# Optimization experiments

Measured on AMD Instinct MI355X. Metric: run time of the kernel, lower is better.

The kernel has to match this reference:

```python
import jax, jax.numpy as jnp
import numpy as np

B, T, V, D, H = 64, 256, 32000, 512, 1024  # batch, seq_len, vocab, word_dim, hidden/embed_dim


def setup_inputs() -> dict:
    key = jax.random.key(0)
    ks = jax.random.split(key, 7)
    tokens = jax.random.randint(ks[0], (B, T), 0, V, dtype=jnp.int64)
    lengths = jnp.maximum(1, jax.random.randint(ks[1], (B,), 0, T + 1, dtype=jnp.int64))
    embedding = jax.random.normal(ks[2], (V, D), dtype=jnp.float32) * 0.05
    W_ih = jax.random.normal(ks[3], (4 * H, D), dtype=jnp.float32) * 0.05
    W_hh = jax.random.normal(ks[4], (4 * H, H), dtype=jnp.float32) * 0.05
    b_ih = jax.random.normal(ks[5], (4 * H,), dtype=jnp.float32) * 0.05
    b_hh = jax.random.normal(ks[6], (4 * H,), dtype=jnp.float32) * 0.05
    return {"tokens": tokens, "lengths": lengths, "embedding": embedding,
            "W_ih": W_ih, "W_hh": W_hh, "b_ih": b_ih, "b_hh": b_hh}


def _lstm_encode(tokens, lengths, embedding, W_ih, W_hh, b_ih, b_hh):
    b, t = tokens.shape
    x = embedding[tokens]                       # [B, T, D] token embedding lookup
    xs = jnp.swapaxes(x, 0, 1)                  # [T, B, D] time-major for scan
    mask = jnp.arange(t)[:, None] < lengths[None, :]  # [T, B] valid-step mask

    h0 = jnp.zeros((b, W_hh.shape[1]), dtype=x.dtype)
    c0 = jnp.zeros_like(h0)

    def step(carry, inp):
        h, c = carry
        xt, mt = inp
        # torch LSTMCell: gates = x W_ih^T + b_ih + h W_hh^T + b_hh, chunk order i, f, g, o
        gates = xt @ W_ih.T + b_ih + h @ W_hh.T + b_hh
        i, f, g, o = jnp.split(gates, 4, axis=-1)
        i = jax.nn.sigmoid(i)
        f = jax.nn.sigmoid(f)
        g = jnp.tanh(g)
        o = jax.nn.sigmoid(o)
        c_new = f * c + i * g
        h_new = o * jnp.tanh(c_new)
        m = mt[:, None]
        # freeze state past each sequence's length -> final h is h at t = length
        h = jnp.where(m, h_new, h)
        c = jnp.where(m, c_new, c)
        return (h, c), None

    (h, c), _ = jax.lax.scan(step, (h0, c0), (xs, mask))
    return h  # [B, H] final hidden state


def reference(tokens, lengths, embedding, W_ih, W_hh, b_ih, b_hh):
    return _lstm_encode(tokens, lengths, embedding, W_ih, W_hh, b_ih, b_hh)
```

## Files before the change

kernel.cpp:

```cpp
#include <hip/hip_runtime.h>


typedef __attribute__((ext_vector_type(8))) short    sh8;
typedef __attribute__((ext_vector_type(4))) float    fx4;
typedef __attribute__((ext_vector_type(4))) unsigned ux4;

__device__ __forceinline__ unsigned short f2bf(float x) {
  unsigned u = __builtin_bit_cast(unsigned, x);
  return (unsigned short)((u + 0x7FFFu + ((u >> 16) & 1u)) >> 16);
}
__device__ __forceinline__ float bf2f(unsigned short s) {
  return __builtin_bit_cast(float, (unsigned)s << 16);
}
__device__ __forceinline__ float sigm(float x) { return 1.0f / (1.0f + __expf(-x)); }
__device__ __forceinline__ float tanh_(float x) { return 2.0f / (1.0f + __expf(-2.0f * x)) - 1.0f; }

__device__ __forceinline__ void ld_sc(sh8& v, const void* p) {
  asm volatile("global_load_dwordx4 %0, %1, off sc0 sc1" : "=v"(v) : "v"(p) : "memory");
}
__device__ __forceinline__ void ld_sc4u(ux4& v, const void* p) {
  asm volatile("global_load_dwordx4 %0, %1, off sc0 sc1" : "=v"(v) : "v"(p) : "memory");
}
__device__ __forceinline__ void st_sc2(void* p, unsigned v) {
  asm volatile("global_store_short %0, %1, off sc0 sc1" :: "v"(p), "v"(v) : "memory");
}
__device__ __forceinline__ void st_sc4(void* p, unsigned v) {
  asm volatile("global_store_dword %0, %1, off sc0 sc1" :: "v"(p), "v"(v) : "memory");
}


__global__ void k_convert(const float* __restrict__ src, ushort* __restrict__ dst, int n4) {
  int i = blockIdx.x * blockDim.x + threadIdx.x;
  int stride = gridDim.x * blockDim.x;
  for (; i < n4; i += stride) {
    float4 v = ((const float4*)src)[i];
    ((ushort4*)dst)[i] = make_ushort4(f2bf(v.x), f2bf(v.y), f2bf(v.z), f2bf(v.w));
  }
}

__global__ void k_bias(const float* __restrict__ bi, const float* __restrict__ bh,
                       float* __restrict__ bias) {
  int i = blockIdx.x * 256 + threadIdx.x;
  if (i < 4096) bias[i] = bi[i] + bh[i];
}

__global__ void k_gather(const int* __restrict__ tokens, const float* __restrict__ emb,
                         ushort* __restrict__ X) {
  int m = blockIdx.x * 4 + (threadIdx.x >> 6);
  int lane = threadIdx.x & 63;
  int b = m & 63, tt = m >> 6;
  int tok = tokens[b * 256 + tt];
  const float4* src = (const float4*)(emb + (size_t)tok * 512);
  ushort4* dst = (ushort4*)(X + (size_t)m * 512);
#pragma unroll
  for (int i = 0; i < 2; ++i) {
    float4 v = src[lane + i * 64];
    dst[lane + i * 64] = make_ushort4(f2bf(v.x), f2bf(v.y), f2bf(v.z), f2bf(v.w));
  }
}


__global__ __launch_bounds__(256) void k1_gemm(const ushort* __restrict__ X,
                                               const ushort* __restrict__ W,
                                               const float* __restrict__ bias,
                                               ushort* __restrict__ Xg) {
  __shared__ __align__(16) char As[128 * 128];
  __shared__ __align__(16) char Bs[128 * 128];
  const int tid = threadIdx.x, lane = tid & 63, wid = tid >> 6;
  const int wm = wid & 1, wn = wid >> 1;
  const int m0 = blockIdx.y * 128, n0 = blockIdx.x * 128;

  fx4 acc[4][4] = {};

  for (int kt = 0; kt < 8; ++kt) {
    if (kt) __syncthreads();
#pragma unroll
    for (int i = 0; i < 4; ++i) {
      int a = tid * 16 + i * 4096;
      int row = a >> 7, inrow = a & 127;
      int dsa = (row << 7) + (inrow ^ ((row & 7) << 4));
      sh8 va = *(const sh8*)((const char*)X + (size_t)(m0 + row) * 1024 + kt * 128 + inrow);
      *(sh8*)(As + dsa) = va;
      sh8 vb = *(const sh8*)((const char*)W + (size_t)(n0 + row) * 1024 + kt * 128 + inrow);
      *(sh8*)(Bs + dsa) = vb;
    }
    __syncthreads();
#pragma unroll
    for (int kb = 0; kb < 2; ++kb) {
      sh8 af[4], bf[4];
      const int ko = kb * 64 + ((lane >> 4) << 4);
#pragma unroll
      for (int x = 0; x < 4; ++x) {
        int ar = wm * 64 + x * 16 + (lane & 15);
        af[x] = *(const sh8*)(As + (ar << 7) + (ko ^ ((ar & 7) << 4)));
        int br = wn * 64 + x * 16 + (lane & 15);
        bf[x] = *(const sh8*)(Bs + (br << 7) + (ko ^ ((br & 7) << 4)));
      }
#pragma unroll
      for (int mi = 0; mi < 4; ++mi)
#pragma unroll
        for (int ni = 0; ni < 4; ++ni)
          acc[mi][ni] = __builtin_amdgcn_mfma_f32_16x16x32_bf16(af[mi], bf[ni], acc[mi][ni], 0, 0, 0);
    }
  }
#pragma unroll
  for (int ni = 0; ni < 4; ++ni) {
    int n = n0 + wn * 64 + ni * 16 + (lane & 15);
    float bv = bias[n];
#pragma unroll
    for (int mi = 0; mi < 4; ++mi) {
#pragma unroll
      for (int r = 0; r < 4; ++r) {
        int m = m0 + wm * 64 + mi * 16 + ((lane >> 4) << 2) + r;
        Xg[(size_t)m * 4096 + n] = f2bf(acc[mi][ni][r] + bv);
      }
    }
  }
}


__global__ __launch_bounds__(256, 1) void k2_lstm(const ushort* __restrict__ Whh,
                                                  const ushort* __restrict__ Xg,
                                                  const int* __restrict__ lengths,
                                                  ushort* __restrict__ hbuf,
                                                  unsigned* __restrict__ flags,
                                                  float* __restrict__ out) {
  __shared__ __align__(16) char hs[32768];
  __shared__ float gs[16][65];

  const int tid = threadIdx.x, lane = tid & 63, wn = tid >> 6;
  const int wg = blockIdx.x;
  const int hidx = wg & 63, beta = wg >> 6;

  const int grow = wn * 1024 + hidx * 16 + (lane & 15);
  sh8 wf[32];
  {
    const char* wsrc = (const char*)Whh + (size_t)grow * 2048 + ((lane >> 4) << 4);
#pragma unroll
    for (int kb = 0; kb < 32; ++kb) {
      wf[kb] = *(const sh8*)(wsrc + (kb << 6));
      asm volatile("" : "+v"(wf[kb]));
    }
  }

  const int b_loc = tid >> 4, j16 = tid & 15;
  const int bglob = beta * 16 + b_loc;
  const int len = lengths[bglob];
  float h_s = 0.0f, c_s = 0.0f;

  const int arow = lane & 15;
  const char* abase = hs + (arow << 11);
  const int asw = (arow & 7) << 4;
  const int ahi = (lane >> 4) << 4;

  const ushort* x0 = Xg + (size_t)bglob * 4096 + hidx * 16 + j16;
  ushort xcu0 = x0[0], xcu1 = x0[1024], xcu2 = x0[2048], xcu3 = x0[3072];

  unsigned* const myflag = flags + beta * 256 + hidx * 4 + wn;
  const char* const fpoll = (const char*)(flags + beta * 256) + lane * 16;

  for (int t = 0; t < 256; ++t) {
    if (t > 0) {
      if (wn == 0) {
        const unsigned tgt = (unsigned)t;
        for (;;) {
          ux4 f;
          ld_sc4u(f, fpoll);
          asm volatile("s_waitcnt vmcnt(0)" ::: "memory");
          unsigned m01 = f[0] < f[1] ? f[0] : f[1];
          unsigned m23 = f[2] < f[3] ? f[2] : f[3];
          unsigned m = m01 < m23 ? m01 : m23;
          if (__all(m >= tgt)) break;
        }
      }
      __syncthreads();
    }

    const char* hbase = (const char*)hbuf + (size_t)(t & 1) * 131072 + (size_t)beta * 32768;
    sh8 st[8];
#pragma unroll
    for (int i = 0; i < 8; ++i) ld_sc(st[i], hbase + tid * 16 + i * 4096);
    asm volatile("s_waitcnt vmcnt(0)" ::: "memory");
    __builtin_amdgcn_sched_barrier(0);
#pragma unroll
    for (int i = 0; i < 8; ++i) {
      int a = tid * 16 + i * 4096;
      int row = a >> 11, inrow = a & 2047;
      *(sh8*)(hs + (row << 11) + (inrow ^ ((row & 7) << 4))) = st[i];
    }
    __syncthreads();

    const int tn = (t + 1) & 255;
    const ushort* xn = Xg + (size_t)tn * 262144 + (size_t)bglob * 4096 + hidx * 16 + j16;
    ushort nx0 = xn[0], nx1 = xn[1024], nx2 = xn[2048], nx3 = xn[3072];

    fx4 ac0 = {0,0,0,0}, ac1 = {0,0,0,0}, ac2 = {0,0,0,0}, ac3 = {0,0,0,0};
#pragma unroll
    for (int kb = 0; kb < 8; ++kb) {
      sh8 a0 = *(const sh8*)(abase + ((((4*kb+0) << 6) + ahi) ^ asw));
      ac0 = __builtin_amdgcn_mfma_f32_16x16x32_bf16(a0, wf[4*kb+0], ac0, 0, 0, 0);
      sh8 a1 = *(const sh8*)(abase + ((((4*kb+1) << 6) + ahi) ^ asw));
      ac1 = __builtin_amdgcn_mfma_f32_16x16x32_bf16(a1, wf[4*kb+1], ac1, 0, 0, 0);
      sh8 a2 = *(const sh8*)(abase + ((((4*kb+2) << 6) + ahi) ^ asw));
      ac2 = __builtin_amdgcn_mfma_f32_16x16x32_bf16(a2, wf[4*kb+2], ac2, 0, 0, 0);
      sh8 a3 = *(const sh8*)(abase + ((((4*kb+3) << 6) + ahi) ^ asw));
      ac3 = __builtin_amdgcn_mfma_f32_16x16x32_bf16(a3, wf[4*kb+3], ac3, 0, 0, 0);
    }
    fx4 acc = (ac0 + ac1) + (ac2 + ac3);

    {
      const int gr = (lane >> 4) << 2;
      const int gc = wn * 16 + (lane & 15);
#pragma unroll
      for (int r = 0; r < 4; ++r) gs[gr + r][gc] = acc[r];
    }
    __syncthreads();

    {
      float gi = gs[b_loc][ 0 + j16] + bf2f(xcu0);
      float gf = gs[b_loc][16 + j16] + bf2f(xcu1);
      float gg = gs[b_loc][32 + j16] + bf2f(xcu2);
      float go = gs[b_loc][48 + j16] + bf2f(xcu3);
      if (t < len) {
        float iv = sigm(gi), fv = sigm(gf), gv = tanh_(gg), ov = sigm(go);
        c_s = fv * c_s + iv * gv;
        h_s = ov * tanh_(c_s);
      }
    }

    {
      char* dst = (char*)hbuf + (size_t)((t + 1) & 1) * 131072 +
                  (size_t)bglob * 2048 + (size_t)(hidx * 16 + j16) * 2;
      st_sc2(dst, (unsigned)f2bf(h_s));
    }
    asm volatile("s_waitcnt vmcnt(0)" ::: "memory");
    if (lane == 0) st_sc4(myflag, (unsigned)(t + 1));

    xcu0 = nx0; xcu1 = nx1; xcu2 = nx2; xcu3 = nx3;
  }

  out[(size_t)bglob * 1024 + hidx * 16 + j16] = h_s;
}


extern "C" void kernel_launch(void* const* d_in, const int* in_sizes, int n_in,
                              void* d_out, int out_size, void* d_ws, size_t ws_size,
                              hipStream_t stream) {
  (void)in_sizes; (void)n_in; (void)out_size;
  const int*   tokens  = (const int*)  d_in[0];
  const int*   lengths = (const int*)  d_in[1];
  const float* emb     = (const float*)d_in[2];
  const float* W_ih    = (const float*)d_in[3];
  const float* W_hh    = (const float*)d_in[4];
  const float* b_ih    = (const float*)d_in[5];
  const float* b_hh    = (const float*)d_in[6];
  float* out = (float*)d_out;
  char* ws = (char*)d_ws;

  const size_t off_X    = 0;
  const size_t off_Wih  = off_X    + (size_t)16384 * 512 * 2;
  const size_t off_Whh  = off_Wih  + (size_t)4096 * 512 * 2;
  const size_t off_bias = off_Whh  + (size_t)4096 * 1024 * 2;
  const size_t off_Xg   = off_bias + (size_t)4096 * 4;
  const size_t off_hbuf = off_Xg   + (size_t)16384 * 4096 * 2;
  const size_t off_flag = off_hbuf + (size_t)2 * 64 * 1024 * 2;
  const size_t need     = off_flag + 4096;
  if (ws_size < need) return;

  ushort*   Xb    = (ushort*)(ws + off_X);
  ushort*   Wih_b = (ushort*)(ws + off_Wih);
  ushort*   Whh_b = (ushort*)(ws + off_Whh);
  float*    bias  = (float*) (ws + off_bias);
  ushort*   Xg    = (ushort*)(ws + off_Xg);
  ushort*   hb    = (ushort*)(ws + off_hbuf);
  unsigned* flags = (unsigned*)(ws + off_flag);

  hipMemsetAsync(ws + off_hbuf, 0, (size_t)2 * 64 * 1024 * 2 + 4096, stream);
  k_convert<<<1024, 256, 0, stream>>>(W_ih, Wih_b, 4096 * 512 / 4);
  k_convert<<<1024, 256, 0, stream>>>(W_hh, Whh_b, 4096 * 1024 / 4);
  k_bias<<<16, 256, 0, stream>>>(b_ih, b_hh, bias);
  k_gather<<<4096, 256, 0, stream>>>(tokens, emb, Xb);
  k1_gemm<<<dim3(32, 128), 256, 0, stream>>>(Xb, Wih_b, bias, Xg);
  k2_lstm<<<256, 256, 0, stream>>>(Whh_b, Xg, lengths, hb, flags, out);
}
```

Baseline: 1.079 ms.

## Replace flag-based grid barrier with step-tagged hidden-state words

Each hidden value is now published as a 32-bit word that packs the bf16 h with a 16-bit step tag. Consumers poll the h buffer itself until every tag matches the current step. This removes the separate flag store, the vmcnt wait before it, and the flag-poll round trip plus __syncthreads before loading h. In exchange the exchanged data doubles in size, and every thread spins on 16 dwordx4 loads instead of one wave polling a small flag array.

```diff
diff --git a/kernel.cpp b/kernel.cpp
--- a/kernel.cpp
+++ b/kernel.cpp
@@ -4,6 +4,7 @@
 typedef __attribute__((ext_vector_type(8))) short    sh8;
 typedef __attribute__((ext_vector_type(4))) float    fx4;
 typedef __attribute__((ext_vector_type(4))) unsigned ux4;
+typedef __attribute__((ext_vector_type(2))) unsigned ux2;
 
 __device__ __forceinline__ unsigned short f2bf(float x) {
   unsigned u = __builtin_bit_cast(unsigned, x);
@@ -15,14 +16,8 @@
 __device__ __forceinline__ float sigm(float x) { return 1.0f / (1.0f + __expf(-x)); }
 __device__ __forceinline__ float tanh_(float x) { return 2.0f / (1.0f + __expf(-2.0f * x)) - 1.0f; }
 
-__device__ __forceinline__ void ld_sc(sh8& v, const void* p) {
-  asm volatile("global_load_dwordx4 %0, %1, off sc0 sc1" : "=v"(v) : "v"(p) : "memory");
-}
 __device__ __forceinline__ void ld_sc4u(ux4& v, const void* p) {
   asm volatile("global_load_dwordx4 %0, %1, off sc0 sc1" : "=v"(v) : "v"(p) : "memory");
-}
-__device__ __forceinline__ void st_sc2(void* p, unsigned v) {
-  asm volatile("global_store_short %0, %1, off sc0 sc1" :: "v"(p), "v"(v) : "memory");
 }
 __device__ __forceinline__ void st_sc4(void* p, unsigned v) {
   asm volatile("global_store_dword %0, %1, off sc0 sc1" :: "v"(p), "v"(v) : "memory");
@@ -122,8 +117,7 @@
 __global__ __launch_bounds__(256, 1) void k2_lstm(const ushort* __restrict__ Whh,
                                                   const ushort* __restrict__ Xg,
                                                   const int* __restrict__ lengths,
-                                                  ushort* __restrict__ hbuf,
-                                                  unsigned* __restrict__ flags,
+                                                  unsigned* __restrict__ hbufT,
                                                   float* __restrict__ out) {
   __shared__ __align__(16) char hs[32768];
   __shared__ float gs[16][65];
@@ -153,40 +147,36 @@
   const int asw = (arow & 7) << 4;
   const int ahi = (lane >> 4) << 4;
 
+  const char* const stage0 = (const char*)hbufT + (size_t)beta * 65536 + tid * 16;
+  const char* const stage1 = stage0 + 262144;
+  unsigned* const pub0 = hbufT + (size_t)bglob * 1024 + hidx * 16 + j16;
+  unsigned* const pub1 = pub0 + 65536;
+
   const ushort* x0 = Xg + (size_t)bglob * 4096 + hidx * 16 + j16;
   ushort xcu0 = x0[0], xcu1 = x0[1024], xcu2 = x0[2048], xcu3 = x0[3072];
 
-  unsigned* const myflag = flags + beta * 256 + hidx * 4 + wn;
-  const char* const fpoll = (const char*)(flags + beta * 256) + lane * 16;
-
   for (int t = 0; t < 256; ++t) {
-    if (t > 0) {
-      if (wn == 0) {
-        const unsigned tgt = (unsigned)t;
-        for (;;) {
-          ux4 f;
-          ld_sc4u(f, fpoll);
-          asm volatile("s_waitcnt vmcnt(0)" ::: "memory");
-          unsigned m01 = f[0] < f[1] ? f[0] : f[1];
-          unsigned m23 = f[2] < f[3] ? f[2] : f[3];
-          unsigned m = m01 < m23 ? m01 : m23;
-          if (__all(m >= tgt)) break;
-        }
-      }
-      __syncthreads();
-    }
-
-    const char* hbase = (const char*)hbuf + (size_t)(t & 1) * 131072 + (size_t)beta * 32768;
-    sh8 st[8];
-#pragma unroll
-    for (int i = 0; i < 8; ++i) ld_sc(st[i], hbase + tid * 16 + i * 4096);
-    asm volatile("s_waitcnt vmcnt(0)" ::: "memory");
-    __builtin_amdgcn_sched_barrier(0);
-#pragma unroll
-    for (int i = 0; i < 8; ++i) {
-      int a = tid * 16 + i * 4096;
-      int row = a >> 11, inrow = a & 2047;
-      *(sh8*)(hs + (row << 11) + (inrow ^ ((row & 7) << 4))) = st[i];
+    const char* sb = (t & 1) ? stage1 : stage0;
+    const unsigned tag = (unsigned)t;
+    ux4 L[16];
+    for (;;) {
+#pragma unroll
+      for (int i = 0; i < 16; ++i) ld_sc4u(L[i], sb + i * 4096);
+      asm volatile("s_waitcnt vmcnt(0)" ::: "memory");
+      unsigned diff = 0;
+#pragma unroll
+      for (int i = 0; i < 16; ++i) {
+        diff |= (L[i][0] ^ tag); diff |= (L[i][1] ^ tag);
+        diff |= (L[i][2] ^ tag); diff |= (L[i][3] ^ tag);
+      }
+      if (__all((diff & 0xFFFFu) == 0u)) break;
+    }
+#pragma unroll
+    for (int i = 0; i < 16; ++i) {
+      ux2 p;
+      p[0] = (L[i][0] >> 16) | (L[i][1] & 0xFFFF0000u);
+      p[1] = (L[i][2] >> 16) | (L[i][3] & 0xFFFF0000u);
+      *(ux2*)(hs + (i << 11) + ((tid * 8) ^ ((i & 7) << 4))) = p;
     }
     __syncthreads();
 
@@ -229,12 +219,9 @@
     }
 
     {
-      char* dst = (char*)hbuf + (size_t)((t + 1) & 1) * 131072 +
-                  (size_t)bglob * 2048 + (size_t)(hidx * 16 + j16) * 2;
-      st_sc2(dst, (unsigned)f2bf(h_s));
-    }
-    asm volatile("s_waitcnt vmcnt(0)" ::: "memory");
-    if (lane == 0) st_sc4(myflag, (unsigned)(t + 1));
+      unsigned v = ((unsigned)f2bf(h_s) << 16) | (unsigned)(t + 1);
+      st_sc4((t & 1) ? pub0 : pub1, v);
+    }
 
     xcu0 = nx0; xcu1 = nx1; xcu2 = nx2; xcu3 = nx3;
   }
@@ -262,9 +249,8 @@
   const size_t off_Whh  = off_Wih  + (size_t)4096 * 512 * 2;
   const size_t off_bias = off_Whh  + (size_t)4096 * 1024 * 2;
   const size_t off_Xg   = off_bias + (size_t)4096 * 4;
-  const size_t off_hbuf = off_Xg   + (size_t)16384 * 4096 * 2;
-  const size_t off_flag = off_hbuf + (size_t)2 * 64 * 1024 * 2;
-  const size_t need     = off_flag + 4096;
+  const size_t off_hbT  = off_Xg   + (size_t)16384 * 4096 * 2;
+  const size_t need     = off_hbT + (size_t)2 * 64 * 1024 * 4;
   if (ws_size < need) return;
 
   ushort*   Xb    = (ushort*)(ws + off_X);
@@ -272,14 +258,13 @@
   ushort*   Whh_b = (ushort*)(ws + off_Whh);
   float*    bias  = (float*) (ws + off_bias);
   ushort*   Xg    = (ushort*)(ws + off_Xg);
-  ushort*   hb    = (ushort*)(ws + off_hbuf);
-  unsigned* flags = (unsigned*)(ws + off_flag);
-
-  hipMemsetAsync(ws + off_hbuf, 0, (size_t)2 * 64 * 1024 * 2 + 4096, stream);
+  unsigned* hbT   = (unsigned*)(ws + off_hbT);
+
+  hipMemsetAsync(ws + off_hbT, 0, (size_t)2 * 64 * 1024 * 4, stream);
   k_convert<<<1024, 256, 0, stream>>>(W_ih, Wih_b, 4096 * 512 / 4);
   k_convert<<<1024, 256, 0, stream>>>(W_hh, Whh_b, 4096 * 1024 / 4);
   k_bias<<<16, 256, 0, stream>>>(b_ih, b_hh, bias);
   k_gather<<<4096, 256, 0, stream>>>(tokens, emb, Xb);
   k1_gemm<<<dim3(32, 128), 256, 0, stream>>>(Xb, Wih_b, bias, Xg);
-  k2_lstm<<<256, 256, 0, stream>>>(Whh_b, Xg, lengths, hb, flags, out);
-}
+  k2_lstm<<<256, 256, 0, stream>>>(Whh_b, Xg, lengths, hbT, out);
+}
```

Measured after the change: 886.2 us. 1.22x faster.
